# Performance work log

Measured on AMD Instinct MI355X. Metric: run time of the kernel, lower is better.

The kernel has to match this reference:

```python
import jax, jax.numpy as jnp
import numpy as np

N = 100000  # number of graph nodes
E = 1600000  # number of edges
EPS = 1e-12  # F.normalize eps


def _l2_normalize(x):
    # F.normalize(x): row-wise L2 normalize with eps clamp
    n = jnp.sqrt(jnp.sum(x * x, axis=1, keepdims=True))
    return x / jnp.maximum(n, EPS)


def setup_inputs() -> dict:
    key = jax.random.key(0)
    ks = jax.random.split(key, 8)
    edges = jax.random.randint(ks[0], (E, 2), 0, N, dtype=jnp.int64 if jax.config.jax_enable_x64 else jnp.int32)
    feat = jax.random.normal(ks[1], (N, 300), dtype=jnp.float32)
    label_idx = jax.random.randint(ks[2], (1000,), 0, N, dtype=jnp.int32)
    # xavier_uniform for weights, zeros for bias (per GraphConv init)
    lim1 = float(np.sqrt(6.0 / (300 + 64)))
    lim2 = float(np.sqrt(6.0 / (64 + 64)))
    w1 = jax.random.uniform(ks[3], (300, 64), jnp.float32, -lim1, lim1)
    b1 = jnp.zeros((64,), jnp.float32)
    w2 = jax.random.uniform(ks[4], (64, 64), jnp.float32, -lim2, lim2)
    b2 = jnp.zeros((64,), jnp.float32)
    return {"edges": edges, "feat": feat, "label_idx": label_idx,
            "w1": w1, "b1": b1, "w2": w2, "b2": b2}


def reference(edges, feat, label_idx, w1, b1, w2, b2):
    # normt_spm(adj, method='in'): transpose adjacency then row-normalize by degree
    # original coo entries are (src=edges[:,0], dst=edges[:,1]); after transpose:
    rows = edges[:, 1]
    cols = edges[:, 0]
    ones = jnp.ones((edges.shape[0],), feat.dtype)
    deg = jax.ops.segment_sum(ones, rows, num_segments=N)  # [N]
    inv_deg = jnp.where(deg > 0, 1.0 / deg, 0.0)

    def spmm(h):
        # (D^-1 A^T) @ h via gather + segment_sum, h: [N, d]
        msg = h[cols] * inv_deg[rows][:, None]  # [E, d]
        return jax.ops.segment_sum(msg, rows, num_segments=N)

    x = feat
    for w, b in ((w1, b1), (w2, b2)):
        # GraphConv: adj @ (x @ w) + b, then LeakyReLU(0.2); dropout inactive (eval)
        x = spmm(x @ w) + b
        x = jax.nn.leaky_relu(x, negative_slope=0.2)
        x = _l2_normalize(x)
    return x[label_idx]
```

## Files before the change

### kernel.cpp

```cpp
#include <hip/hip_runtime.h>

#define N_NODES 100000
#define N_EDGES 1600000
#define FEAT_D 300
#define HID_D 64
#define SCAN_NB 98

__global__ void hist_kernel(const int* __restrict__ edges, int* __restrict__ cnt) {
    int e = blockIdx.x * blockDim.x + threadIdx.x;
    if (e < N_EDGES) atomicAdd(&cnt[edges[2 * e + 1]], 1);
}

__global__ void invdeg_kernel(const int* __restrict__ cnt, float* __restrict__ invdeg) {
    int i = blockIdx.x * blockDim.x + threadIdx.x;
    if (i < N_NODES) {
        int d = cnt[i];
        invdeg[i] = d > 0 ? 1.f / (float)d : 0.f;
    }
}

__global__ void scan1_kernel(const int* __restrict__ cnt, int* __restrict__ rp,
                             int* __restrict__ bsum) {
    __shared__ int sh[256];
    int base = blockIdx.x * 1024 + threadIdx.x * 4;
    int v[4];
    int s = 0;
#pragma unroll
    for (int j = 0; j < 4; ++j) {
        int idx = base + j;
        v[j] = (idx < N_NODES) ? cnt[idx] : 0;
        s += v[j];
    }
    sh[threadIdx.x] = s;
    __syncthreads();
    for (int off = 1; off < 256; off <<= 1) {
        int t = (threadIdx.x >= off) ? sh[threadIdx.x - off] : 0;
        __syncthreads();
        sh[threadIdx.x] += t;
        __syncthreads();
    }
    int excl = sh[threadIdx.x] - s;
    if (threadIdx.x == 255) bsum[blockIdx.x] = sh[255];
#pragma unroll
    for (int j = 0; j < 4; ++j) {
        int idx = base + j;
        if (idx < N_NODES) rp[idx] = excl;
        excl += v[j];
    }
}

__global__ void scan2_kernel(int* __restrict__ bsum, int* __restrict__ rp) {
    if (threadIdx.x == 0 && blockIdx.x == 0) {
        int acc = 0;
        for (int i = 0; i < SCAN_NB; ++i) {
            int t = bsum[i];
            bsum[i] = acc;
            acc += t;
        }
        rp[N_NODES] = acc;
    }
}

__global__ void scan3_kernel(int* __restrict__ rp, const int* __restrict__ bsum) {
    int base = blockIdx.x * 1024 + threadIdx.x * 4;
    int add = bsum[blockIdx.x];
#pragma unroll
    for (int j = 0; j < 4; ++j) {
        int idx = base + j;
        if (idx < N_NODES) rp[idx] += add;
    }
}

__global__ void scatter_kernel(const int* __restrict__ edges, const int* __restrict__ rp,
                               int* __restrict__ cursor, int* __restrict__ csr_col) {
    int e = blockIdx.x * blockDim.x + threadIdx.x;
    if (e < N_EDGES) {
        int row = edges[2 * e + 1];
        int p = rp[row] + atomicAdd(&cursor[row], 1);
        csr_col[p] = edges[2 * e];
    }
}

template <int K, int KC>
__global__ __launch_bounds__(256) void gemm_kernel(const float* __restrict__ x,
                                                   const float* __restrict__ w,
                                                   float* __restrict__ out) {
    constexpr int XP = 68;
    constexpr int F4R = KC / 4;
    constexpr int NCH = K / KC;
    constexpr int NX = (128 * F4R + 255) / 256;
    constexpr int NW = (KC * 16 + 255) / 256;
    __shared__ __align__(16) float xS[128 * XP];
    __shared__ __align__(16) float wS[KC * 64];

    const int tid = threadIdx.x;
    const int g = tid >> 3;
    const int c8 = (tid & 7) * 8;
    const long r0 = (long)blockIdx.x * 128;

    float acc[4][8];
#pragma unroll
    for (int i = 0; i < 4; ++i)
#pragma unroll
        for (int j = 0; j < 8; ++j) acc[i][j] = 0.f;

    float4 pfx[NX];
    float4 pfw[NW];

    auto issue = [&](int k0) {
#pragma unroll
        for (int l = 0; l < NX; ++l) {
            int i = tid + l * 256;
            pfx[l] = make_float4(0.f, 0.f, 0.f, 0.f);
            if (i < 128 * F4R) {
                int r = i / F4R, m = i % F4R;
                long gr = r0 + r;
                if (gr < N_NODES) pfx[l] = *(const float4*)(x + gr * K + k0 + 4 * m);
            }
        }
#pragma unroll
        for (int l = 0; l < NW; ++l) {
            int i = tid + l * 256;
            if (i < KC * 16) pfw[l] = ((const float4*)(w + (long)k0 * 64))[i];
        }
    };
    auto commit = [&]() {
#pragma unroll
        for (int l = 0; l < NX; ++l) {
            int i = tid + l * 256;
            if (i < 128 * F4R) {
                int r = i / F4R, m = i % F4R;
                *(float4*)&xS[r * XP + 4 * m] = pfx[l];
            }
        }
#pragma unroll
        for (int l = 0; l < NW; ++l) {
            int i = tid + l * 256;
            if (i < KC * 16) ((float4*)wS)[i] = pfw[l];
        }
    };

    issue(0);
    commit();
    __syncthreads();

    for (int c = 0; c < NCH; ++c) {
        if (c + 1 < NCH) issue((c + 1) * KC);
#pragma unroll 3
        for (int k = 0; k < KC; k += 4) {
            float4 xv[4];
#pragma unroll
            for (int i = 0; i < 4; ++i)
                xv[i] = *(const float4*)&xS[(g + 32 * i) * XP + k];
#pragma unroll
            for (int kk = 0; kk < 4; ++kk) {
                float4 wa = *(const float4*)&wS[(k + kk) * 64 + c8];
                float4 wb = *(const float4*)&wS[(k + kk) * 64 + c8 + 4];
#pragma unroll
                for (int i = 0; i < 4; ++i) {
                    float xi = ((const float*)&xv[i])[kk];
                    acc[i][0] = fmaf(xi, wa.x, acc[i][0]);
                    acc[i][1] = fmaf(xi, wa.y, acc[i][1]);
                    acc[i][2] = fmaf(xi, wa.z, acc[i][2]);
                    acc[i][3] = fmaf(xi, wa.w, acc[i][3]);
                    acc[i][4] = fmaf(xi, wb.x, acc[i][4]);
                    acc[i][5] = fmaf(xi, wb.y, acc[i][5]);
                    acc[i][6] = fmaf(xi, wb.z, acc[i][6]);
                    acc[i][7] = fmaf(xi, wb.w, acc[i][7]);
                }
            }
        }
        __syncthreads();
        if (c + 1 < NCH) {
            commit();
            __syncthreads();
        }
    }

#pragma unroll
    for (int i = 0; i < 4; ++i) {
        long gr = r0 + g + 32 * i;
        if (gr < N_NODES) {
            *(float4*)(out + gr * 64 + c8) =
                make_float4(acc[i][0], acc[i][1], acc[i][2], acc[i][3]);
            *(float4*)(out + gr * 64 + c8 + 4) =
                make_float4(acc[i][4], acc[i][5], acc[i][6], acc[i][7]);
        }
    }
}

__global__ void spmm_fused_kernel(const int* __restrict__ rp, const int* __restrict__ csr_col,
                                  const float* __restrict__ invdeg, const float* __restrict__ h,
                                  const float* __restrict__ b, float* __restrict__ out) {
    int row = blockIdx.x * 4 + (threadIdx.x >> 6);
    int lane = threadIdx.x & 63;
    int sub = lane >> 4;
    int f4 = (lane & 15) * 4;
    int s = rp[row], e = rp[row + 1];

    float4 acc = make_float4(0.f, 0.f, 0.f, 0.f);
    int i = s + sub;
    for (; i + 4 < e; i += 8) {
        int c0 = csr_col[i];
        int c1 = csr_col[i + 4];
        float4 v0 = *(const float4*)(h + (long)c0 * 64 + f4);
        float4 v1 = *(const float4*)(h + (long)c1 * 64 + f4);
        acc.x += v0.x + v1.x;
        acc.y += v0.y + v1.y;
        acc.z += v0.z + v1.z;
        acc.w += v0.w + v1.w;
    }
    if (i < e) {
        int c0 = csr_col[i];
        float4 v0 = *(const float4*)(h + (long)c0 * 64 + f4);
        acc.x += v0.x;
        acc.y += v0.y;
        acc.z += v0.z;
        acc.w += v0.w;
    }

    acc.x += __shfl_xor(acc.x, 16);
    acc.y += __shfl_xor(acc.y, 16);
    acc.z += __shfl_xor(acc.z, 16);
    acc.w += __shfl_xor(acc.w, 16);
    acc.x += __shfl_xor(acc.x, 32);
    acc.y += __shfl_xor(acc.y, 32);
    acc.z += __shfl_xor(acc.z, 32);
    acc.w += __shfl_xor(acc.w, 32);

    float id = invdeg[row];
    float4 bb = *(const float4*)(b + f4);
    float4 v;
    v.x = acc.x * id + bb.x;
    v.y = acc.y * id + bb.y;
    v.z = acc.z * id + bb.z;
    v.w = acc.w * id + bb.w;
    v.x = v.x >= 0.f ? v.x : 0.2f * v.x;
    v.y = v.y >= 0.f ? v.y : 0.2f * v.y;
    v.z = v.z >= 0.f ? v.z : 0.2f * v.z;
    v.w = v.w >= 0.f ? v.w : 0.2f * v.w;

    float ss = v.x * v.x + v.y * v.y + v.z * v.z + v.w * v.w;
    ss += __shfl_xor(ss, 1);
    ss += __shfl_xor(ss, 2);
    ss += __shfl_xor(ss, 4);
    ss += __shfl_xor(ss, 8);
    float inv = 1.f / fmaxf(sqrtf(ss), 1e-12f);

    if (sub == 0) {
        v.x *= inv;
        v.y *= inv;
        v.z *= inv;
        v.w *= inv;
        *(float4*)(out + (long)row * 64 + f4) = v;
    }
}

__global__ void gather_kernel(const float* __restrict__ x, const int* __restrict__ idx,
                              float* __restrict__ out) {
    int i = blockIdx.x * blockDim.x + threadIdx.x;
    if (i < 1000 * 64) {
        int r = i >> 6;
        out[i] = x[(long)idx[r] * 64 + (i & 63)];
    }
}

extern "C" void kernel_launch(void* const* d_in, const int* in_sizes, int n_in,
                              void* d_out, int out_size, void* d_ws, size_t ws_size,
                              hipStream_t stream) {
    const int* edges = (const int*)d_in[0];
    const float* feat = (const float*)d_in[1];
    const int* label_idx = (const int*)d_in[2];
    const float* w1 = (const float*)d_in[3];
    const float* b1 = (const float*)d_in[4];
    const float* w2 = (const float*)d_in[5];
    const float* b2 = (const float*)d_in[6];
    float* out = (float*)d_out;

    int* cnt = (int*)d_ws;
    int* cursor = cnt + 100352;
    int* rp = cursor + 100352;
    int* bsum = rp + 100416;
    float* invdeg = (float*)(bsum + 128);
    int* csr_col = (int*)(invdeg + 100352);
    float* bufA = (float*)(csr_col + 1600000);
    float* bufB = bufA + (long)N_NODES * 64;

    hipMemsetAsync(cnt, 0, 2 * 100352 * sizeof(int), stream);
    hist_kernel<<<(N_EDGES + 255) / 256, 256, 0, stream>>>(edges, cnt);
    invdeg_kernel<<<(N_NODES + 255) / 256, 256, 0, stream>>>(cnt, invdeg);
    scan1_kernel<<<SCAN_NB, 256, 0, stream>>>(cnt, rp, bsum);
    scan2_kernel<<<1, 64, 0, stream>>>(bsum, rp);
    scan3_kernel<<<SCAN_NB, 256, 0, stream>>>(rp, bsum);
    scatter_kernel<<<(N_EDGES + 255) / 256, 256, 0, stream>>>(edges, rp, cursor, csr_col);

    const int gemm_blocks = (N_NODES + 127) / 128;

    gemm_kernel<FEAT_D, 60><<<gemm_blocks, 256, 0, stream>>>(feat, w1, bufA);
    spmm_fused_kernel<<<N_NODES / 4, 256, 0, stream>>>(rp, csr_col, invdeg, bufA, b1, bufB);

    gemm_kernel<HID_D, 64><<<gemm_blocks, 256, 0, stream>>>(bufB, w2, bufA);
    spmm_fused_kernel<<<N_NODES / 4, 256, 0, stream>>>(rp, csr_col, invdeg, bufA, b2, bufB);

    gather_kernel<<<(1000 * 64 + 255) / 256, 256, 0, stream>>>(bufB, label_idx, out);
}
```

Baseline: 572.0 us.

## Replace FP32 FMA GEMMs with split-bf16 MFMA (3-pass) GEMMs

Replaces the scalar FP32 register-tiled GEMM with a matrix-core kernel. Each FP32 value is split into high and low bf16 halves, and three bf16 MFMA products (hi*hi, hi*lo, lo*hi) approximate FP32 accuracy. The weights are pre-split and transposed by a small new kernel, while the activations are split on the fly into shared memory. This trades extra conversion work and three MFMA passes for far higher matrix throughput on the feature-projection GEMM, at some precision risk.

```diff
diff --git a/kernel.cpp b/kernel.cpp
--- a/kernel.cpp
+++ b/kernel.cpp
@@ -5,6 +5,20 @@
 #define FEAT_D 300
 #define HID_D 64
 #define SCAN_NB 98
+
+typedef __attribute__((ext_vector_type(8))) short short8;
+typedef __attribute__((ext_vector_type(4))) float f32x4;
+typedef unsigned int u32;
+typedef unsigned short u16;
+
+__device__ inline void split2(float v, u16& h, u16& l) {
+    u32 u = __float_as_uint(v);
+    h = (u16)(u >> 16);
+    float lo = v - __uint_as_float(u & 0xffff0000u);
+    u32 lu = __float_as_uint(lo);
+    lu += 0x7fffu + ((lu >> 16) & 1u);
+    l = (u16)(lu >> 16);
+}
 
 __global__ void hist_kernel(const int* __restrict__ edges, int* __restrict__ cnt) {
     int e = blockIdx.x * blockDim.x + threadIdx.x;
@@ -81,110 +95,121 @@
     }
 }
 
-template <int K, int KC>
-__global__ __launch_bounds__(256) void gemm_kernel(const float* __restrict__ x,
-                                                   const float* __restrict__ w,
-                                                   float* __restrict__ out) {
-    constexpr int XP = 68;
-    constexpr int F4R = KC / 4;
-    constexpr int NCH = K / KC;
-    constexpr int NX = (128 * F4R + 255) / 256;
-    constexpr int NW = (KC * 16 + 255) / 256;
-    __shared__ __align__(16) float xS[128 * XP];
-    __shared__ __align__(16) float wS[KC * 64];
+__global__ void wsplit_kernel(const float* __restrict__ w, u16* __restrict__ wtH,
+                              u16* __restrict__ wtL, int K, int KW) {
+    int id = blockIdx.x * blockDim.x + threadIdx.x;
+    if (id >= 64 * KW) return;
+    int c = id / KW, k = id % KW;
+    float v = (k < K) ? w[(long)k * 64 + c] : 0.f;
+    u16 h, l;
+    split2(v, h, l);
+    wtH[(long)c * KW + k] = h;
+    wtL[(long)c * KW + k] = l;
+}
+
+template <int K, int KW>
+__global__ __launch_bounds__(256) void gemm_mfma(const float* __restrict__ x,
+                                                 const u16* __restrict__ wtH,
+                                                 const u16* __restrict__ wtL,
+                                                 float* __restrict__ out) {
+    constexpr int NCH = (K + 31) / 32;
+    constexpr int RS = 40;
+    __shared__ __align__(16) u16 aH[128 * RS];
+    __shared__ __align__(16) u16 aL[128 * RS];
 
     const int tid = threadIdx.x;
-    const int g = tid >> 3;
-    const int c8 = (tid & 7) * 8;
+    const int lane = tid & 63;
+    const int wm = tid >> 6;
+    const int l15 = lane & 15;
+    const int lg = lane >> 4;
     const long r0 = (long)blockIdx.x * 128;
 
-    float acc[4][8];
-#pragma unroll
-    for (int i = 0; i < 4; ++i)
-#pragma unroll
-        for (int j = 0; j < 8; ++j) acc[i][j] = 0.f;
-
-    float4 pfx[NX];
-    float4 pfw[NW];
-
-    auto issue = [&](int k0) {
-#pragma unroll
-        for (int l = 0; l < NX; ++l) {
-            int i = tid + l * 256;
-            pfx[l] = make_float4(0.f, 0.f, 0.f, 0.f);
-            if (i < 128 * F4R) {
-                int r = i / F4R, m = i % F4R;
-                long gr = r0 + r;
-                if (gr < N_NODES) pfx[l] = *(const float4*)(x + gr * K + k0 + 4 * m);
+    f32x4 acc[2][4];
+#pragma unroll
+    for (int i = 0; i < 2; ++i)
+#pragma unroll
+        for (int j = 0; j < 4; ++j)
+#pragma unroll
+            for (int e = 0; e < 4; ++e) acc[i][j][e] = 0.f;
+
+    const int sr = tid >> 3;
+    const int sm = tid & 7;
+    float4 pf[4];
+
+    auto issueA = [&](int k0) {
+#pragma unroll
+        for (int l = 0; l < 4; ++l) {
+            long gr = r0 + sr + 32 * l;
+            float4 v = make_float4(0.f, 0.f, 0.f, 0.f);
+            bool kok = (K % 32 == 0) || (k0 + 4 * sm + 3 < K);
+            if (gr < N_NODES && kok) v = *(const float4*)(x + gr * K + k0 + 4 * sm);
+            pf[l] = v;
+        }
+    };
+    auto commitA = [&]() {
+#pragma unroll
+        for (int l = 0; l < 4; ++l) {
+            int r = sr + 32 * l;
+            u16 h0, h1, h2, h3, q0, q1, q2, q3;
+            split2(pf[l].x, h0, q0);
+            split2(pf[l].y, h1, q1);
+            split2(pf[l].z, h2, q2);
+            split2(pf[l].w, h3, q3);
+            uint2 ph = make_uint2((u32)h0 | ((u32)h1 << 16), (u32)h2 | ((u32)h3 << 16));
+            uint2 pl = make_uint2((u32)q0 | ((u32)q1 << 16), (u32)q2 | ((u32)q3 << 16));
+            *(uint2*)&aH[r * RS + 4 * sm] = ph;
+            *(uint2*)&aL[r * RS + 4 * sm] = pl;
+        }
+    };
+
+    issueA(0);
+    commitA();
+    __syncthreads();
+
+    for (int c = 0; c < NCH; ++c) {
+        const int k0 = c * 32;
+        if (c + 1 < NCH) issueA(k0 + 32);
+
+        short8 bh[4], bl[4];
+#pragma unroll
+        for (int ct = 0; ct < 4; ++ct) {
+            long off = (long)(ct * 16 + l15) * KW + k0 + lg * 8;
+            bh[ct] = *(const short8*)(wtH + off);
+            bl[ct] = *(const short8*)(wtL + off);
+        }
+        short8 ah[2], al[2];
+#pragma unroll
+        for (int rt = 0; rt < 2; ++rt) {
+            int row = wm * 32 + rt * 16 + l15;
+            ah[rt] = *(const short8*)&aH[row * RS + lg * 8];
+            al[rt] = *(const short8*)&aL[row * RS + lg * 8];
+        }
+#pragma unroll
+        for (int rt = 0; rt < 2; ++rt)
+#pragma unroll
+            for (int ct = 0; ct < 4; ++ct) {
+                acc[rt][ct] = __builtin_amdgcn_mfma_f32_16x16x32_bf16(ah[rt], bh[ct], acc[rt][ct], 0, 0, 0);
+                acc[rt][ct] = __builtin_amdgcn_mfma_f32_16x16x32_bf16(ah[rt], bl[ct], acc[rt][ct], 0, 0, 0);
+                acc[rt][ct] = __builtin_amdgcn_mfma_f32_16x16x32_bf16(al[rt], bh[ct], acc[rt][ct], 0, 0, 0);
             }
-        }
-#pragma unroll
-        for (int l = 0; l < NW; ++l) {
-            int i = tid + l * 256;
-            if (i < KC * 16) pfw[l] = ((const float4*)(w + (long)k0 * 64))[i];
-        }
-    };
-    auto commit = [&]() {
-#pragma unroll
-        for (int l = 0; l < NX; ++l) {
-            int i = tid + l * 256;
-            if (i < 128 * F4R) {
-                int r = i / F4R, m = i % F4R;
-                *(float4*)&xS[r * XP + 4 * m] = pfx[l];
-            }
-        }
-#pragma unroll
-        for (int l = 0; l < NW; ++l) {
-            int i = tid + l * 256;
-            if (i < KC * 16) ((float4*)wS)[i] = pfw[l];
-        }
-    };
-
-    issue(0);
-    commit();
-    __syncthreads();
-
-    for (int c = 0; c < NCH; ++c) {
-        if (c + 1 < NCH) issue((c + 1) * KC);
-#pragma unroll 3
-        for (int k = 0; k < KC; k += 4) {
-            float4 xv[4];
-#pragma unroll
-            for (int i = 0; i < 4; ++i)
-                xv[i] = *(const float4*)&xS[(g + 32 * i) * XP + k];
-#pragma unroll
-            for (int kk = 0; kk < 4; ++kk) {
-                float4 wa = *(const float4*)&wS[(k + kk) * 64 + c8];
-                float4 wb = *(const float4*)&wS[(k + kk) * 64 + c8 + 4];
-#pragma unroll
-                for (int i = 0; i < 4; ++i) {
-                    float xi = ((const float*)&xv[i])[kk];
-                    acc[i][0] = fmaf(xi, wa.x, acc[i][0]);
-                    acc[i][1] = fmaf(xi, wa.y, acc[i][1]);
-                    acc[i][2] = fmaf(xi, wa.z, acc[i][2]);
-                    acc[i][3] = fmaf(xi, wa.w, acc[i][3]);
-                    acc[i][4] = fmaf(xi, wb.x, acc[i][4]);
-                    acc[i][5] = fmaf(xi, wb.y, acc[i][5]);
-                    acc[i][6] = fmaf(xi, wb.z, acc[i][6]);
-                    acc[i][7] = fmaf(xi, wb.w, acc[i][7]);
-                }
-            }
-        }
         __syncthreads();
         if (c + 1 < NCH) {
-            commit();
+            commitA();
             __syncthreads();
         }
     }
 
 #pragma unroll
-    for (int i = 0; i < 4; ++i) {
-        long gr = r0 + g + 32 * i;
-        if (gr < N_NODES) {
-            *(float4*)(out + gr * 64 + c8) =
-                make_float4(acc[i][0], acc[i][1], acc[i][2], acc[i][3]);
-            *(float4*)(out + gr * 64 + c8 + 4) =
-                make_float4(acc[i][4], acc[i][5], acc[i][6], acc[i][7]);
+    for (int rt = 0; rt < 2; ++rt) {
+        int rbase = wm * 32 + rt * 16 + lg * 4;
+#pragma unroll
+        for (int reg = 0; reg < 4; ++reg) {
+            long gr = r0 + rbase + reg;
+            if (gr < N_NODES) {
+#pragma unroll
+                for (int ct = 0; ct < 4; ++ct)
+                    out[gr * 64 + ct * 16 + l15] = acc[rt][ct][reg];
+            }
         }
     }
 }
@@ -285,8 +310,14 @@
     int* csr_col = (int*)(invdeg + 100352);
     float* bufA = (float*)(csr_col + 1600000);
     float* bufB = bufA + (long)N_NODES * 64;
+    u16* wt1H = (u16*)(bufB + (long)N_NODES * 64);
+    u16* wt1L = wt1H + 64 * 320;
+    u16* wt2H = wt1L + 64 * 320;
+    u16* wt2L = wt2H + 64 * 64;
 
     hipMemsetAsync(cnt, 0, 2 * 100352 * sizeof(int), stream);
+    wsplit_kernel<<<(64 * 320 + 255) / 256, 256, 0, stream>>>(w1, wt1H, wt1L, 300, 320);
+    wsplit_kernel<<<(64 * 64 + 255) / 256, 256, 0, stream>>>(w2, wt2H, wt2L, 64, 64);
     hist_kernel<<<(N_EDGES + 255) / 256, 256, 0, stream>>>(edges, cnt);
     invdeg_kernel<<<(N_NODES + 255) / 256, 256, 0, stream>>>(cnt, invdeg);
     scan1_kernel<<<SCAN_NB, 256, 0, stream>>>(cnt, rp, bsum);
@@ -296,10 +327,10 @@
 
     const int gemm_blocks = (N_NODES + 127) / 128;
 
-    gemm_kernel<FEAT_D, 60><<<gemm_blocks, 256, 0, stream>>>(feat, w1, bufA);
+    gemm_mfma<FEAT_D, 320><<<gemm_blocks, 256, 0, stream>>>(feat, wt1H, wt1L, bufA);
     spmm_fused_kernel<<<N_NODES / 4, 256, 0, stream>>>(rp, csr_col, invdeg, bufA, b1, bufB);
 
-    gemm_kernel<HID_D, 64><<<gemm_blocks, 256, 0, stream>>>(bufB, w2, bufA);
+    gemm_mfma<HID_D, 64><<<gemm_blocks, 256, 0, stream>>>(bufB, wt2H, wt2L, bufA);
     spmm_fused_kernel<<<N_NODES / 4, 256, 0, stream>>>(rp, csr_col, invdeg, bufA, b2, bufB);
 
     gather_kernel<<<(1000 * 64 + 255) / 256, 256, 0, stream>>>(bufB, label_idx, out);
```

After: 521.4 us. -8.8%, faster.
